# Performance work log

Measured on AMD Instinct MI355X. Metric: run time of the kernel, lower is better.

The kernel has to match this reference:

```python
import jax, jax.numpy as jnp
import numpy as np

B, C, N = 4, 512, 4096
CH = C // 2  # query/key projection dim


def setup_inputs() -> dict:
    key = jax.random.key(0)
    ks = jax.random.split(key, 10)
    s = 1.0 / np.sqrt(C)
    return {
        "Q": jax.random.normal(ks[0], (B, C, N), dtype=jnp.float32),
        "K": jax.random.normal(ks[1], (B, C, N), dtype=jnp.float32),
        "V": jax.random.normal(ks[2], (B, C, N), dtype=jnp.float32),
        "Wq": jax.random.normal(ks[3], (CH, C), dtype=jnp.float32) * s,
        "bq": jax.random.normal(ks[4], (CH,), dtype=jnp.float32) * s,
        "Wk": jax.random.normal(ks[5], (CH, C), dtype=jnp.float32) * s,
        "bk": jax.random.normal(ks[6], (CH,), dtype=jnp.float32) * s,
        "Wv": jax.random.normal(ks[7], (C, C), dtype=jnp.float32) * s,
        "bv": jax.random.normal(ks[8], (C,), dtype=jnp.float32) * s,
        "gamma": jnp.full((1,), 0.5, dtype=jnp.float32),  # torch inits to 0; nonzero for meaningful math
    }


def reference(Q, K, V, Wq, bq, Wk, bk, Wv, bv, gamma):
    # Conv1d(kernel_size=1) == per-position linear over channels
    q = jnp.einsum("oc,bcn->bon", Wq, Q) + bq[None, :, None]  # [B, C/2, N]
    k = jnp.einsum("oc,bcn->bon", Wk, K) + bk[None, :, None]  # [B, C/2, N]
    v = jnp.einsum("oc,bcn->bon", Wv, V) + bv[None, :, None]  # [B, C, N]
    # energy[b,n,m] = <q[b,:,n], k[b,:,m]>  (no 1/sqrt(d) scaling in original)
    energy = jnp.einsum("bcn,bcm->bnm", q, k)                 # [B, N, N]
    attention = jax.nn.softmax(energy, axis=-1)
    # out[b,c,n] = sum_m v[b,c,m] * attention[b,n,m]
    out = jnp.einsum("bcm,bnm->bcn", v, attention)            # [B, C, N]
    return gamma * out + V
```

## Files before the change

### kernel.cpp

```cpp
#include <hip/hip_runtime.h>
#include <cstdint>
#include <cstddef>

constexpr int B_  = 4;
constexpr int C_  = 512;
constexpr int CH_ = 256;
constexpr int N_  = 4096;
#define LOG2E 1.4426950408889634f

typedef float    f32x4 __attribute__((ext_vector_type(4)));
typedef _Float16 f16x8 __attribute__((ext_vector_type(8)));
typedef _Float16 f16x4 __attribute__((ext_vector_type(4)));

__device__ __forceinline__ f32x4 MFMA16(f16x8 a, f16x8 b, f32x4 c) {
  return __builtin_amdgcn_mfma_f32_16x16x32_f16(a, b, c, 0, 0, 0);
}

typedef const __attribute__((address_space(1))) unsigned int* gas_u32p;
typedef __attribute__((address_space(3))) unsigned int* las_u32p;
__device__ __forceinline__ void async16(const void* g, void* l) {
  __builtin_amdgcn_global_load_lds((gas_u32p)g, (las_u32p)l, 16, 0, 0);
}

template <int CTRL>
__device__ __forceinline__ float dppmax(float x) {
  float y = __builtin_bit_cast(
      float, __builtin_amdgcn_update_dpp(0, __builtin_bit_cast(int, x), CTRL,
                                         0xF, 0xF, true));
  return fmaxf(x, y);
}
__device__ __forceinline__ float rowmax16(float x) {
  x = dppmax<0x128>(x); x = dppmax<0x124>(x);
  x = dppmax<0x122>(x); x = dppmax<0x121>(x);
  return x;
}

__global__ void prep_w_kernel(const float* __restrict__ Wq,
                              const float* __restrict__ Wk,
                              const float* __restrict__ Wv,
                              _Float16* __restrict__ wq,
                              _Float16* __restrict__ wk,
                              _Float16* __restrict__ wv) {
  int i = blockIdx.x * 256 + threadIdx.x;
  if (i < CH_ * C_) {
    wq[i] = (_Float16)(Wq[i] * LOG2E);
    wk[i] = (_Float16)Wk[i];
  }
  if (i < C_ * C_) wv[i] = (_Float16)Wv[i];
}

__global__ __launch_bounds__(512, 4) void proj_kernel(
    const _Float16* __restrict__ wq, const _Float16* __restrict__ wk,
    const _Float16* __restrict__ wv, const float* __restrict__ Q,
    const float* __restrict__ K, const float* __restrict__ V,
    const float* __restrict__ bq, const float* __restrict__ bk,
    const float* __restrict__ bv, _Float16* __restrict__ qT,
    _Float16* __restrict__ kT, _Float16* __restrict__ vT) {
  __shared__ __align__(16) _Float16 lW[2][256 * 32];
  __shared__ __align__(16) _Float16 lX[2][64 * 56];

  const int y = blockIdx.y;
  const _Float16* W;
  const float* X;
  const float* bias;
  _Float16* out;
  int o0 = 0, M, mode;
  float bscale = 1.0f;
  if (y == 0) {
    W = wq; X = Q; bias = bq; out = qT; M = CH_; mode = 0; bscale = LOG2E;
  } else if (y == 1) {
    W = wk; X = K; bias = bk; out = kT; M = CH_; mode = 0;
  } else {
    W = wv; X = V; bias = bv; out = vT; M = C_; mode = 1; o0 = (y - 2) * 256;
  }

  const int tid = threadIdx.x;
  const int lane = tid & 63, wave = tid >> 6;
  const int g = lane >> 4, lm = lane & 15;
  const int b = blockIdx.z;
  const int n0 = blockIdx.x * 64;
  const int wo = (wave >> 1) * 64, wn = (wave & 1) * 32;

  const _Float16* Wb = W + (size_t)o0 * C_;
  const float* Xb = X + (size_t)b * C_ * N_;

  f32x4 acc[8];
#pragma unroll
  for (int i = 0; i < 8; ++i) acc[i] = f32x4{0.f, 0.f, 0.f, 0.f};

  auto stageW = [&](int s, int buf) {
    int c0 = s * 32;
#pragma unroll
    for (int r = 0; r < 2; ++r) {
      int ci = r * 512 + tid;
      int o = ci >> 2, cg = ci & 3;
      async16(Wb + (size_t)o * C_ + c0 + cg * 8,
              (char*)&lW[buf][0] + r * 8192 + wave * 1024);
    }
  };

  const int xc = tid >> 4;
  const int xn4 = (tid & 15) * 4;
  const int xgran = xc >> 3, xcin = xc & 7;
  auto gloadX = [&](int s) {
    return *(const f32x4*)(Xb + (size_t)(s * 32 + xc) * N_ + n0 + xn4);
  };
  auto writeX = [&](int buf, f32x4 v) {
#pragma unroll
    for (int i = 0; i < 4; ++i) {
      int n = xn4 + i;
      int pos = (xgran ^ ((n >> 2) & 3)) * 8 + xcin;
      lX[buf][n * 56 + pos] = (_Float16)v[i];
    }
  };

  f32x4 xg = gloadX(0);
  writeX(0, xg);
  xg = gloadX(1);
  stageW(0, 0);
  __syncthreads();

#pragma unroll
  for (int s = 0; s < 16; ++s) {
    const int cb = s & 1, nb = cb ^ 1;
    if (s < 15) stageW(s + 1, nb);
    f32x4 xgn;
    if (s < 14) xgn = gloadX(s + 2);

    f16x8 wf[4], xf[2];
#pragma unroll
    for (int ot = 0; ot < 4; ++ot)
      wf[ot] = *(const f16x8*)&lW[cb][((wo + ot * 16 + lm) * 4 + g) * 8];
#pragma unroll
    for (int nt = 0; nt < 2; ++nt) {
      int n = wn + nt * 16 + lm;
      int pos = (g ^ ((n >> 2) & 3)) * 8;
      xf[nt] = *(const f16x8*)&lX[cb][n * 56 + pos];
    }

    if (mode == 0) {
#pragma unroll
      for (int nt = 0; nt < 2; ++nt)
#pragma unroll
        for (int ot = 0; ot < 4; ++ot)
          acc[nt * 4 + ot] = MFMA16(xf[nt], wf[ot], acc[nt * 4 + ot]);
    } else {
#pragma unroll
      for (int ot = 0; ot < 4; ++ot)
#pragma unroll
        for (int nt = 0; nt < 2; ++nt)
          acc[ot * 2 + nt] = MFMA16(wf[ot], xf[nt], acc[ot * 2 + nt]);
    }

    if (s < 15) writeX(nb, xg);
    if (s < 14) xg = xgn;
    __syncthreads();
  }

  if (mode == 0) {
#pragma unroll
    for (int nt = 0; nt < 2; ++nt) {
#pragma unroll
      for (int ot = 0; ot < 4; ++ot) {
        int o = wo + ot * 16 + lm;
        float bv_ = bias[o] * bscale;
#pragma unroll
        for (int r = 0; r < 4; ++r) {
          int n = n0 + wn + nt * 16 + g * 4 + r;
          out[((size_t)b * N_ + n) * M + o] =
              (_Float16)(acc[nt * 4 + ot][r] + bv_);
        }
      }
    }
  } else {
#pragma unroll
    for (int ot = 0; ot < 4; ++ot) {
#pragma unroll
      for (int r = 0; r < 4; ++r) {
        int o = o0 + wo + ot * 16 + g * 4 + r;
        float bv_ = bias[o];
#pragma unroll
        for (int nt = 0; nt < 2; ++nt) {
          int n = n0 + wn + nt * 16 + lm;
          out[((size_t)b * M + o) * N_ + n] =
              (_Float16)(acc[ot * 2 + nt][r] + bv_);
        }
      }
    }
  }
}

__global__ __launch_bounds__(512, 2) void attn_kernel(
    const _Float16* __restrict__ qT, const _Float16* __restrict__ kT,
    const _Float16* __restrict__ vT, float* __restrict__ Op0,
    _Float16* __restrict__ Op1, float* __restrict__ mbuf,
    float* __restrict__ lbuf) {
  __shared__ __align__(16) _Float16 kstage[2 * 8192];
  __shared__ __align__(16) _Float16 P_t[128 * 72];
  __shared__ float al_st[128];
  __shared__ int bumped[8];

  const int tid = threadIdx.x;
  const int lane = tid & 63, wave = tid >> 6;
  const int g = lane >> 4, lm = lane & 15;

  const int bx = blockIdx.x;
  const int xcd = bx & 7;
  const int b = xcd >> 1, h = xcd & 1;
  const int n0 = (bx >> 3) * 128;
  const int mbase = h * 2048;
  const int c0w = wave * 64;

  f32x4 O[4][8];
#pragma unroll
  for (int i = 0; i < 4; ++i)
#pragma unroll
    for (int j = 0; j < 8; ++j) O[i][j] = f32x4{0.f, 0.f, 0.f, 0.f};
  f32x4 Ol = f32x4{0.f, 0.f, 0.f, 0.f};

  const _Float16* qTb = qT + ((size_t)b * N_ + n0) * CH_;
  f16x8 qf[8];
#pragma unroll
  for (int p = 0; p < 2; ++p) {
#pragma unroll
    for (int r = 0; r < 4; ++r) {
      int sidx = r * 512 + tid;
      int rl = sidx >> 5, cgs = sidx & 31;
      async16(qTb + (size_t)(p * 64 + rl) * CH_ + ((cgs ^ (rl & 7)) * 8),
              (char*)kstage + r * 8192 + wave * 1024);
    }
    __syncthreads();
    if ((wave >> 2) == p) {
      int rl = (wave & 3) * 16 + lm;
#pragma unroll
      for (int ks = 0; ks < 8; ++ks)
        qf[ks] =
            *(const f16x8*)&kstage[rl * 256 + (((ks * 4 + g) ^ (rl & 7)) * 8)];
    }
    __syncthreads();
  }

  const _Float16* kTb = kT + ((size_t)b * N_ + mbase) * CH_;
  auto stage_k = [&](int it) {
    int m0 = it * 32;
    char* dst0 = (char*)kstage + (it & 1) * 16384;
#pragma unroll
    for (int r = 0; r < 2; ++r) {
      int sidx = r * 512 + tid;
      int key = sidx >> 5, cgs = sidx & 31;
      async16(kTb + (size_t)(m0 + key) * CH_ + ((cgs ^ (key & 7)) * 8),
              dst0 + r * 8192 + wave * 1024);
    }
  };
  stage_k(0);

  const _Float16* vTb = vT + (size_t)b * C_ * N_ + mbase;
  const _Float16* vbase[4];
#pragma unroll
  for (int ct = 0; ct < 4; ++ct)
    vbase[ct] = vTb + (size_t)(c0w + ct * 16 + lm) * N_ + g * 8;
  f16x8 vf[4], vfn[4];
#pragma unroll
  for (int ct = 0; ct < 4; ++ct) vf[ct] = *(const f16x8*)vbase[ct];

  f32x4 m_run = f32x4{-1e30f, -1e30f, -1e30f, -1e30f};
  f16x8 ones;
#pragma unroll
  for (int i = 0; i < 8; ++i) ones[i] = (_Float16)1.0f;

#pragma unroll 1
  for (int it = 0; it < 64; ++it) {
    __syncthreads();
    if (it < 63) stage_k(it + 1);

    const _Float16* kb = kstage + (it & 1) * 8192;
    f32x4 s0 = f32x4{0.f, 0.f, 0.f, 0.f};
    f32x4 s1 = f32x4{0.f, 0.f, 0.f, 0.f};
    const int key0 = lm, key1 = 16 + lm;
#pragma unroll
    for (int ks = 0; ks < 8; ++ks) {
      f16x8 kf0 =
          *(const f16x8*)&kb[key0 * 256 + (((ks * 4 + g) ^ (key0 & 7)) * 8)];
      f16x8 kf1 =
          *(const f16x8*)&kb[key1 * 256 + (((ks * 4 + g) ^ (key1 & 7)) * 8)];
      s0 = MFMA16(qf[ks], kf0, s0);
      s1 = MFMA16(qf[ks], kf1, s1);
    }

    f32x4 alpha;
    bool anyb = false;
#pragma unroll
    for (int r = 0; r < 4; ++r) {
      float mx = rowmax16(fmaxf(s0[r], s1[r]));
      float mnew = fmaxf(m_run[r], mx);
      alpha[r] = exp2f(m_run[r] - mnew);
      anyb |= (mnew > m_run[r]);
      m_run[r] = mnew;
      float p0 = exp2f(s0[r] - mnew);
      float p1 = exp2f(s1[r] - mnew);
      int row = wave * 16 + g * 4 + r;
      P_t[row * 72 + lm] = (_Float16)p0;
      P_t[row * 72 + 16 + lm] = (_Float16)p1;
    }
    if (lm == 0) *(f32x4*)&al_st[wave * 16 + g * 4] = alpha;
    unsigned long long bal = __ballot(anyb);
    if (lane == 0) bumped[wave] = (bal != 0ull) ? 1 : 0;
    __syncthreads();

    if (it < 63) {
      int mo = (it + 1) * 32;
#pragma unroll
      for (int ct = 0; ct < 4; ++ct)
        vfn[ct] = *(const f16x8*)(vbase[ct] + mo);
    }

#pragma unroll
    for (int nt = 0; nt < 8; ++nt) {
      if (__builtin_amdgcn_readfirstlane(bumped[nt])) {
        float a = al_st[nt * 16 + lm];
#pragma unroll
        for (int ct = 0; ct < 4; ++ct) {
          O[ct][nt][0] *= a; O[ct][nt][1] *= a;
          O[ct][nt][2] *= a; O[ct][nt][3] *= a;
        }
      }
    }
    if (__builtin_amdgcn_readfirstlane(bumped[wave])) {
      float a = al_st[wave * 16 + lm];
      Ol[0] *= a; Ol[1] *= a; Ol[2] *= a; Ol[3] *= a;
    }

#pragma unroll
    for (int nt = 0; nt < 8; ++nt) {
      f16x8 pf = *(const f16x8*)&P_t[(nt * 16 + lm) * 72 + g * 8];
#pragma unroll
      for (int ct = 0; ct < 4; ++ct) O[ct][nt] = MFMA16(vf[ct], pf, O[ct][nt]);
    }
    {
      f16x8 pfo = *(const f16x8*)&P_t[(wave * 16 + lm) * 72 + g * 8];
      Ol = MFMA16(ones, pfo, Ol);
    }
    if (it < 63) {
#pragma unroll
      for (int ct = 0; ct < 4; ++ct) vf[ct] = vfn[ct];
    }
  }

  const size_t hb = (size_t)(b * 2 + h) * N_ + n0;
  if (lm == 0) {
#pragma unroll
    for (int r = 0; r < 4; ++r) mbuf[hb + wave * 16 + g * 4 + r] = m_run[r];
  }
  if (lane < 16) lbuf[hb + wave * 16 + lane] = Ol[0];

  if (h == 0) {
    float* ob = Op0 + (size_t)b * C_ * N_;
#pragma unroll
    for (int nt = 0; nt < 8; ++nt) {
      int n_g = n0 + nt * 16 + lm;
#pragma unroll
      for (int ct = 0; ct < 4; ++ct) {
        int cb = c0w + ct * 16 + g * 4;
#pragma unroll
        for (int r = 0; r < 4; ++r)
          ob[(size_t)(cb + r) * N_ + n_g] = O[ct][nt][r];
      }
    }
  } else {
    _Float16* ob = Op1 + (size_t)b * C_ * N_;
#pragma unroll
    for (int nt = 0; nt < 8; ++nt) {
      int n_g = n0 + nt * 16 + lm;
#pragma unroll
      for (int ct = 0; ct < 4; ++ct) {
        int cb = c0w + ct * 16 + g * 4;
#pragma unroll
        for (int r = 0; r < 4; ++r)
          ob[(size_t)(cb + r) * N_ + n_g] = (_Float16)O[ct][nt][r];
      }
    }
  }
}

__global__ __launch_bounds__(256) void combine_kernel(
    float* __restrict__ out, const _Float16* __restrict__ Op1,
    const float* __restrict__ mbuf, const float* __restrict__ lbuf,
    const float* __restrict__ Vin, const float* __restrict__ gptr) {
  const int b = blockIdx.y;
  const int tid = threadIdx.x;
  const int n = blockIdx.x * 64 + (tid & 15) * 4;
  const int cg = tid >> 4;
  const float gamma = gptr[0];

  float s0[4], s1[4];
#pragma unroll
  for (int j = 0; j < 4; ++j) {
    float m0 = mbuf[(size_t)(b * 2 + 0) * N_ + n + j];
    float m1 = mbuf[(size_t)(b * 2 + 1) * N_ + n + j];
    float mx = fmaxf(m0, m1);
    float a0 = exp2f(m0 - mx), a1 = exp2f(m1 - mx);
    float l = a0 * lbuf[(size_t)(b * 2 + 0) * N_ + n + j] +
              a1 * lbuf[(size_t)(b * 2 + 1) * N_ + n + j];
    float inv = gamma / l;
    s0[j] = a0 * inv;
    s1[j] = a1 * inv;
  }

  const _Float16* O1b = Op1 + (size_t)b * C_ * N_;
  for (int c = cg * 32; c < cg * 32 + 32; ++c) {
    size_t idx = ((size_t)b * C_ + c) * N_ + n;
    f32x4 p0 = *(const f32x4*)(out + idx);
    f16x4 p1 = *(const f16x4*)(O1b + (size_t)c * N_ + n);
    f32x4 V = *(const f32x4*)(Vin + idx);
    f32x4 r;
#pragma unroll
    for (int j = 0; j < 4; ++j)
      r[j] = p0[j] * s0[j] + (float)p1[j] * s1[j] + V[j];
    *(f32x4*)(out + idx) = r;
  }
}

extern "C" void kernel_launch(void* const* d_in, const int* in_sizes, int n_in,
                              void* d_out, int out_size, void* d_ws, size_t ws_size,
                              hipStream_t stream) {
  const float* Q  = (const float*)d_in[0];
  const float* K  = (const float*)d_in[1];
  const float* V  = (const float*)d_in[2];
  const float* Wq = (const float*)d_in[3];
  const float* bq = (const float*)d_in[4];
  const float* Wk = (const float*)d_in[5];
  const float* bk = (const float*)d_in[6];
  const float* Wv = (const float*)d_in[7];
  const float* bv = (const float*)d_in[8];
  const float* gm = (const float*)d_in[9];
  float* out = (float*)d_out;

  char* p = (char*)d_ws;
  _Float16* wq = (_Float16*)p; p += (size_t)CH_ * C_ * 2;
  _Float16* wk = (_Float16*)p; p += (size_t)CH_ * C_ * 2;
  _Float16* wv = (_Float16*)p; p += (size_t)C_ * C_ * 2;
  _Float16* qT = (_Float16*)p; p += (size_t)B_ * N_ * CH_ * 2;
  _Float16* kT = (_Float16*)p; p += (size_t)B_ * N_ * CH_ * 2;
  _Float16* vT = (_Float16*)p; p += (size_t)B_ * C_ * N_ * 2;
  _Float16* Op1 = (_Float16*)p; p += (size_t)B_ * C_ * N_ * 2;
  float* mbuf = (float*)p; p += (size_t)B_ * 2 * N_ * 4;
  float* lbuf = (float*)p; p += (size_t)B_ * 2 * N_ * 4;

  prep_w_kernel<<<(C_ * C_) / 256, 256, 0, stream>>>(Wq, Wk, Wv, wq, wk, wv);

  proj_kernel<<<dim3(N_ / 64, 4, B_), 512, 0, stream>>>(
      wq, wk, wv, Q, K, V, bq, bk, bv, qT, kT, vT);

  attn_kernel<<<256, 512, 0, stream>>>(qT, kT, vT, out, Op1, mbuf, lbuf);

  combine_kernel<<<dim3(N_ / 64, B_), 256, 0, stream>>>(out, Op1, mbuf, lbuf,
                                                        V, gm);
}
```

Baseline: 378.5 us.

## Retile attention to 64-query blocks of four waves with lazy max rescaling

The attention kernel now uses 256-thread blocks that each cover 64 query rows, launched as 512 blocks instead of 256. Each wave owns 128 output channels rather than 64. The V register prefetch for the next step is replaced by a direct load in the current iteration. The running-max update only rescales when the new max exceeds the old one by more than 8 (log2 domain), which skips most O rescales. It also wraps the MFMA sections in s_setprio. The cost is more K staging traffic per query, because each K tile is shared by fewer rows, exposed V load latency, and larger unnormalized exponent values that stay within fp16 range.

```diff
diff --git a/kernel.cpp b/kernel.cpp
--- a/kernel.cpp
+++ b/kernel.cpp
@@ -190,15 +190,15 @@
   }
 }
 
-__global__ __launch_bounds__(512, 2) void attn_kernel(
+__global__ __launch_bounds__(256, 2) void attn_kernel(
     const _Float16* __restrict__ qT, const _Float16* __restrict__ kT,
     const _Float16* __restrict__ vT, float* __restrict__ Op0,
     _Float16* __restrict__ Op1, float* __restrict__ mbuf,
     float* __restrict__ lbuf) {
   __shared__ __align__(16) _Float16 kstage[2 * 8192];
-  __shared__ __align__(16) _Float16 P_t[128 * 72];
-  __shared__ float al_st[128];
-  __shared__ int bumped[8];
+  __shared__ __align__(16) _Float16 P_t[64 * 72];
+  __shared__ float al_st[64];
+  __shared__ int bumped[4];
 
   const int tid = threadIdx.x;
   const int lane = tid & 63, wave = tid >> 6;
@@ -207,61 +207,55 @@
   const int bx = blockIdx.x;
   const int xcd = bx & 7;
   const int b = xcd >> 1, h = xcd & 1;
-  const int n0 = (bx >> 3) * 128;
+  const int n0 = (bx >> 3) * 64;
   const int mbase = h * 2048;
-  const int c0w = wave * 64;
-
-  f32x4 O[4][8];
-#pragma unroll
-  for (int i = 0; i < 4; ++i)
-#pragma unroll
-    for (int j = 0; j < 8; ++j) O[i][j] = f32x4{0.f, 0.f, 0.f, 0.f};
+  const int c0w = wave * 128;
+
+  f32x4 O[8][4];
+#pragma unroll
+  for (int i = 0; i < 8; ++i)
+#pragma unroll
+    for (int j = 0; j < 4; ++j) O[i][j] = f32x4{0.f, 0.f, 0.f, 0.f};
   f32x4 Ol = f32x4{0.f, 0.f, 0.f, 0.f};
 
   const _Float16* qTb = qT + ((size_t)b * N_ + n0) * CH_;
   f16x8 qf[8];
 #pragma unroll
-  for (int p = 0; p < 2; ++p) {
-#pragma unroll
-    for (int r = 0; r < 4; ++r) {
-      int sidx = r * 512 + tid;
-      int rl = sidx >> 5, cgs = sidx & 31;
-      async16(qTb + (size_t)(p * 64 + rl) * CH_ + ((cgs ^ (rl & 7)) * 8),
-              (char*)kstage + r * 8192 + wave * 1024);
-    }
-    __syncthreads();
-    if ((wave >> 2) == p) {
-      int rl = (wave & 3) * 16 + lm;
-#pragma unroll
-      for (int ks = 0; ks < 8; ++ks)
-        qf[ks] =
-            *(const f16x8*)&kstage[rl * 256 + (((ks * 4 + g) ^ (rl & 7)) * 8)];
-    }
-    __syncthreads();
-  }
+  for (int r = 0; r < 8; ++r) {
+    int sidx = r * 256 + tid;
+    int rl = sidx >> 5, cgs = sidx & 31;
+    async16(qTb + (size_t)rl * CH_ + ((cgs ^ (rl & 7)) * 8),
+            (char*)kstage + r * 4096 + wave * 1024);
+  }
+  __syncthreads();
+  {
+    int rl = wave * 16 + lm;
+#pragma unroll
+    for (int ks = 0; ks < 8; ++ks)
+      qf[ks] =
+          *(const f16x8*)&kstage[rl * 256 + (((ks * 4 + g) ^ (rl & 7)) * 8)];
+  }
+  __syncthreads();
 
   const _Float16* kTb = kT + ((size_t)b * N_ + mbase) * CH_;
   auto stage_k = [&](int it) {
     int m0 = it * 32;
     char* dst0 = (char*)kstage + (it & 1) * 16384;
 #pragma unroll
-    for (int r = 0; r < 2; ++r) {
-      int sidx = r * 512 + tid;
+    for (int r = 0; r < 4; ++r) {
+      int sidx = r * 256 + tid;
       int key = sidx >> 5, cgs = sidx & 31;
       async16(kTb + (size_t)(m0 + key) * CH_ + ((cgs ^ (key & 7)) * 8),
-              dst0 + r * 8192 + wave * 1024);
+              dst0 + r * 4096 + wave * 1024);
     }
   };
   stage_k(0);
 
   const _Float16* vTb = vT + (size_t)b * C_ * N_ + mbase;
-  const _Float16* vbase[4];
-#pragma unroll
-  for (int ct = 0; ct < 4; ++ct)
-    vbase[ct] = vTb + (size_t)(c0w + ct * 16 + lm) * N_ + g * 8;
-  f16x8 vf[4], vfn[4];
-#pragma unroll
-  for (int ct = 0; ct < 4; ++ct) vf[ct] = *(const f16x8*)vbase[ct];
+  int voff[8];
+#pragma unroll
+  for (int ct = 0; ct < 8; ++ct) voff[ct] = (c0w + ct * 16 + lm) * N_ + g * 8;
+  f16x8 vf[8];
 
   f32x4 m_run = f32x4{-1e30f, -1e30f, -1e30f, -1e30f};
   f16x8 ones;
@@ -277,6 +271,7 @@
     f32x4 s0 = f32x4{0.f, 0.f, 0.f, 0.f};
     f32x4 s1 = f32x4{0.f, 0.f, 0.f, 0.f};
     const int key0 = lm, key1 = 16 + lm;
+    __builtin_amdgcn_s_setprio(1);
 #pragma unroll
     for (int ks = 0; ks < 8; ++ks) {
       f16x8 kf0 =
@@ -286,15 +281,17 @@
       s0 = MFMA16(qf[ks], kf0, s0);
       s1 = MFMA16(qf[ks], kf1, s1);
     }
+    __builtin_amdgcn_s_setprio(0);
 
     f32x4 alpha;
     bool anyb = false;
 #pragma unroll
     for (int r = 0; r < 4; ++r) {
       float mx = rowmax16(fmaxf(s0[r], s1[r]));
-      float mnew = fmaxf(m_run[r], mx);
-      alpha[r] = exp2f(m_run[r] - mnew);
-      anyb |= (mnew > m_run[r]);
+      bool need = (mx > m_run[r] + 8.0f);
+      float mnew = need ? mx : m_run[r];
+      alpha[r] = need ? exp2f(m_run[r] - mnew) : 1.0f;
+      anyb |= need;
       m_run[r] = mnew;
       float p0 = exp2f(s0[r] - mnew);
       float p1 = exp2f(s1[r] - mnew);
@@ -307,19 +304,17 @@
     if (lane == 0) bumped[wave] = (bal != 0ull) ? 1 : 0;
     __syncthreads();
 
-    if (it < 63) {
-      int mo = (it + 1) * 32;
-#pragma unroll
-      for (int ct = 0; ct < 4; ++ct)
-        vfn[ct] = *(const f16x8*)(vbase[ct] + mo);
-    }
-
-#pragma unroll
-    for (int nt = 0; nt < 8; ++nt) {
+    const int mo = it * 32;
+#pragma unroll
+    for (int ct = 0; ct < 8; ++ct)
+      vf[ct] = *(const f16x8*)(vTb + voff[ct] + mo);
+
+#pragma unroll
+    for (int nt = 0; nt < 4; ++nt) {
       if (__builtin_amdgcn_readfirstlane(bumped[nt])) {
         float a = al_st[nt * 16 + lm];
 #pragma unroll
-        for (int ct = 0; ct < 4; ++ct) {
+        for (int ct = 0; ct < 8; ++ct) {
           O[ct][nt][0] *= a; O[ct][nt][1] *= a;
           O[ct][nt][2] *= a; O[ct][nt][3] *= a;
         }
@@ -330,20 +325,18 @@
       Ol[0] *= a; Ol[1] *= a; Ol[2] *= a; Ol[3] *= a;
     }
 
-#pragma unroll
-    for (int nt = 0; nt < 8; ++nt) {
+    __builtin_amdgcn_s_setprio(1);
+#pragma unroll
+    for (int nt = 0; nt < 4; ++nt) {
       f16x8 pf = *(const f16x8*)&P_t[(nt * 16 + lm) * 72 + g * 8];
 #pragma unroll
-      for (int ct = 0; ct < 4; ++ct) O[ct][nt] = MFMA16(vf[ct], pf, O[ct][nt]);
+      for (int ct = 0; ct < 8; ++ct) O[ct][nt] = MFMA16(vf[ct], pf, O[ct][nt]);
     }
     {
       f16x8 pfo = *(const f16x8*)&P_t[(wave * 16 + lm) * 72 + g * 8];
       Ol = MFMA16(ones, pfo, Ol);
     }
-    if (it < 63) {
-#pragma unroll
-      for (int ct = 0; ct < 4; ++ct) vf[ct] = vfn[ct];
-    }
+    __builtin_amdgcn_s_setprio(0);
   }
 
   const size_t hb = (size_t)(b * 2 + h) * N_ + n0;
@@ -356,10 +349,10 @@
   if (h == 0) {
     float* ob = Op0 + (size_t)b * C_ * N_;
 #pragma unroll
-    for (int nt = 0; nt < 8; ++nt) {
+    for (int nt = 0; nt < 4; ++nt) {
       int n_g = n0 + nt * 16 + lm;
 #pragma unroll
-      for (int ct = 0; ct < 4; ++ct) {
+      for (int ct = 0; ct < 8; ++ct) {
         int cb = c0w + ct * 16 + g * 4;
 #pragma unroll
         for (int r = 0; r < 4; ++r)
@@ -369,10 +362,10 @@
   } else {
     _Float16* ob = Op1 + (size_t)b * C_ * N_;
 #pragma unroll
-    for (int nt = 0; nt < 8; ++nt) {
+    for (int nt = 0; nt < 4; ++nt) {
       int n_g = n0 + nt * 16 + lm;
 #pragma unroll
-      for (int ct = 0; ct < 4; ++ct) {
+      for (int ct = 0; ct < 8; ++ct) {
         int cb = c0w + ct * 16 + g * 4;
 #pragma unroll
         for (int r = 0; r < 4; ++r)
@@ -451,7 +444,7 @@
   proj_kernel<<<dim3(N_ / 64, 4, B_), 512, 0, stream>>>(
       wq, wk, wv, Q, K, V, bq, bk, bv, qT, kT, vT);
 
-  attn_kernel<<<256, 512, 0, stream>>>(qT, kT, vT, out, Op1, mbuf, lbuf);
+  attn_kernel<<<512, 256, 0, stream>>>(qT, kT, vT, out, Op1, mbuf, lbuf);
 
   combine_kernel<<<dim3(N_ / 64, B_), 256, 0, stream>>>(out, Op1, mbuf, lbuf,
                                                         V, gm);
```

Result: no change. 384.9 us (+1.7%).

## Software-pipeline attention loop: overlap PV of previous tile with QK of current

Applied to the files above, without the earlier changes.

Double-buffers the P, alpha and bump-flag shared arrays so the PV MFMA for the previous key tile runs after the current tile's QK and softmax. This removes one __syncthreads per iteration and adds a drain step after the loop. It also adds a lazy max-rescale threshold, so the running max is only updated when the new max exceeds it by 8 in log2 units, and s_setprio hints around the MFMA blocks. The lazy rescale could risk fp16 overflow of P values, since they can reach up to 2^8 before being rescaled.

```diff
diff --git a/kernel.cpp b/kernel.cpp
--- a/kernel.cpp
+++ b/kernel.cpp
@@ -196,9 +196,9 @@
     _Float16* __restrict__ Op1, float* __restrict__ mbuf,
     float* __restrict__ lbuf) {
   __shared__ __align__(16) _Float16 kstage[2 * 8192];
-  __shared__ __align__(16) _Float16 P_t[128 * 72];
-  __shared__ float al_st[128];
-  __shared__ int bumped[8];
+  __shared__ __align__(16) _Float16 P_t[2][128 * 72];
+  __shared__ float al_st[2][128];
+  __shared__ int bumped[2][8];
 
   const int tid = threadIdx.x;
   const int lane = tid & 63, wave = tid >> 6;
@@ -255,13 +255,10 @@
   stage_k(0);
 
   const _Float16* vTb = vT + (size_t)b * C_ * N_ + mbase;
-  const _Float16* vbase[4];
-#pragma unroll
-  for (int ct = 0; ct < 4; ++ct)
-    vbase[ct] = vTb + (size_t)(c0w + ct * 16 + lm) * N_ + g * 8;
+  int voff[4];
+#pragma unroll
+  for (int ct = 0; ct < 4; ++ct) voff[ct] = (c0w + ct * 16 + lm) * N_ + g * 8;
   f16x8 vf[4], vfn[4];
-#pragma unroll
-  for (int ct = 0; ct < 4; ++ct) vf[ct] = *(const f16x8*)vbase[ct];
 
   f32x4 m_run = f32x4{-1e30f, -1e30f, -1e30f, -1e30f};
   f16x8 ones;
@@ -273,10 +270,15 @@
     __syncthreads();
     if (it < 63) stage_k(it + 1);
 
+#pragma unroll
+    for (int ct = 0; ct < 4; ++ct)
+      vfn[ct] = *(const f16x8*)(vTb + voff[ct] + it * 32);
+
     const _Float16* kb = kstage + (it & 1) * 8192;
     f32x4 s0 = f32x4{0.f, 0.f, 0.f, 0.f};
     f32x4 s1 = f32x4{0.f, 0.f, 0.f, 0.f};
     const int key0 = lm, key1 = 16 + lm;
+    __builtin_amdgcn_s_setprio(1);
 #pragma unroll
     for (int ks = 0; ks < 8; ++ks) {
       f16x8 kf0 =
@@ -286,38 +288,77 @@
       s0 = MFMA16(qf[ks], kf0, s0);
       s1 = MFMA16(qf[ks], kf1, s1);
     }
-
+    __builtin_amdgcn_s_setprio(0);
+
+    float p0v[4], p1v[4];
     f32x4 alpha;
     bool anyb = false;
 #pragma unroll
     for (int r = 0; r < 4; ++r) {
       float mx = rowmax16(fmaxf(s0[r], s1[r]));
-      float mnew = fmaxf(m_run[r], mx);
-      alpha[r] = exp2f(m_run[r] - mnew);
-      anyb |= (mnew > m_run[r]);
+      bool need = (mx > m_run[r] + 8.0f);
+      float mnew = need ? mx : m_run[r];
+      alpha[r] = need ? exp2f(m_run[r] - mnew) : 1.0f;
+      anyb |= need;
       m_run[r] = mnew;
-      float p0 = exp2f(s0[r] - mnew);
-      float p1 = exp2f(s1[r] - mnew);
+      p0v[r] = exp2f(s0[r] - mnew);
+      p1v[r] = exp2f(s1[r] - mnew);
+    }
+
+    const int pb = (it ^ 1) & 1;
+    if (it) {
+#pragma unroll
+      for (int nt = 0; nt < 8; ++nt) {
+        if (__builtin_amdgcn_readfirstlane(bumped[pb][nt])) {
+          float a = al_st[pb][nt * 16 + lm];
+#pragma unroll
+          for (int ct = 0; ct < 4; ++ct) {
+            O[ct][nt][0] *= a; O[ct][nt][1] *= a;
+            O[ct][nt][2] *= a; O[ct][nt][3] *= a;
+          }
+        }
+      }
+      if (__builtin_amdgcn_readfirstlane(bumped[pb][wave])) {
+        float a = al_st[pb][wave * 16 + lm];
+        Ol[0] *= a; Ol[1] *= a; Ol[2] *= a; Ol[3] *= a;
+      }
+      __builtin_amdgcn_s_setprio(1);
+#pragma unroll
+      for (int nt = 0; nt < 8; ++nt) {
+        f16x8 pf = *(const f16x8*)&P_t[pb][(nt * 16 + lm) * 72 + g * 8];
+#pragma unroll
+        for (int ct = 0; ct < 4; ++ct)
+          O[ct][nt] = MFMA16(vf[ct], pf, O[ct][nt]);
+      }
+      {
+        f16x8 pfo = *(const f16x8*)&P_t[pb][(wave * 16 + lm) * 72 + g * 8];
+        Ol = MFMA16(ones, pfo, Ol);
+      }
+      __builtin_amdgcn_s_setprio(0);
+    }
+
+    const int cb = it & 1;
+#pragma unroll
+    for (int r = 0; r < 4; ++r) {
       int row = wave * 16 + g * 4 + r;
-      P_t[row * 72 + lm] = (_Float16)p0;
-      P_t[row * 72 + 16 + lm] = (_Float16)p1;
-    }
-    if (lm == 0) *(f32x4*)&al_st[wave * 16 + g * 4] = alpha;
+      P_t[cb][row * 72 + lm] = (_Float16)p0v[r];
+      P_t[cb][row * 72 + 16 + lm] = (_Float16)p1v[r];
+    }
+    if (lm == 0) *(f32x4*)&al_st[cb][wave * 16 + g * 4] = alpha;
     unsigned long long bal = __ballot(anyb);
-    if (lane == 0) bumped[wave] = (bal != 0ull) ? 1 : 0;
-    __syncthreads();
-
-    if (it < 63) {
-      int mo = (it + 1) * 32;
-#pragma unroll
-      for (int ct = 0; ct < 4; ++ct)
-        vfn[ct] = *(const f16x8*)(vbase[ct] + mo);
-    }
-
+    if (lane == 0) bumped[cb][wave] = (bal != 0ull) ? 1 : 0;
+
+#pragma unroll
+    for (int ct = 0; ct < 4; ++ct) vf[ct] = vfn[ct];
+  }
+
+  __syncthreads();
+  {
+    const int pb = 1;
 #pragma unroll
     for (int nt = 0; nt < 8; ++nt) {
-      if (__builtin_amdgcn_readfirstlane(bumped[nt])) {
-        float a = al_st[nt * 16 + lm];
+      if (__builtin_amdgcn_readfirstlane(bumped[pb][nt])) {
+        float a = al_st[pb][nt * 16 + lm];
 #pragma unroll
         for (int ct = 0; ct < 4; ++ct) {
           O[ct][nt][0] *= a; O[ct][nt][1] *= a;
@@ -325,24 +366,20 @@
         }
       }
     }
-    if (__builtin_amdgcn_readfirstlane(bumped[wave])) {
-      float a = al_st[wave * 16 + lm];
+    if (__builtin_amdgcn_readfirstlane(bumped[pb][wave])) {
+      float a = al_st[pb][wave * 16 + lm];
       Ol[0] *= a; Ol[1] *= a; Ol[2] *= a; Ol[3] *= a;
     }
-
 #pragma unroll
     for (int nt = 0; nt < 8; ++nt) {
-      f16x8 pf = *(const f16x8*)&P_t[(nt * 16 + lm) * 72 + g * 8];
-#pragma unroll
-      for (int ct = 0; ct < 4; ++ct) O[ct][nt] = MFMA16(vf[ct], pf, O[ct][nt]);
+      f16x8 pf = *(const f16x8*)&P_t[pb][(nt * 16 + lm) * 72 + g * 8];
+#pragma unroll
+      for (int ct = 0; ct < 4; ++ct)
+        O[ct][nt] = MFMA16(vf[ct], pf, O[ct][nt]);
     }
     {
-      f16x8 pfo = *(const f16x8*)&P_t[(wave * 16 + lm) * 72 + g * 8];
+      f16x8 pfo = *(const f16x8*)&P_t[pb][(wave * 16 + lm) * 72 + g * 8];
       Ol = MFMA16(ones, pfo, Ol);
-    }
-    if (it < 63) {
-#pragma unroll
-      for (int ct = 0; ct < 4; ++ct) vf[ct] = vfn[ct];
     }
   }
 
@@ -360,10 +397,10 @@
       int n_g = n0 + nt * 16 + lm;
 #pragma unroll
       for (int ct = 0; ct < 4; ++ct) {
-        int cb = c0w + ct * 16 + g * 4;
+        int cb2 = c0w + ct * 16 + g * 4;
 #pragma unroll
         for (int r = 0; r < 4; ++r)
-          ob[(size_t)(cb + r) * N_ + n_g] = O[ct][nt][r];
+          ob[(size_t)(cb2 + r) * N_ + n_g] = O[ct][nt][r];
       }
     }
   } else {
@@ -373,10 +410,10 @@
       int n_g = n0 + nt * 16 + lm;
 #pragma unroll
       for (int ct = 0; ct < 4; ++ct) {
-        int cb = c0w + ct * 16 + g * 4;
+        int cb2 = c0w + ct * 16 + g * 4;
 #pragma unroll
         for (int r = 0; r < 4; ++r)
-          ob[(size_t)(cb + r) * N_ + n_g] = (_Float16)O[ct][nt][r];
+          ob[(size_t)(cb2 + r) * N_ + n_g] = (_Float16)O[ct][nt][r];
       }
     }
   }
```

Result: slower. 402.1 us (+6.2%).

## Transpose score MFMA and use lazy thresholded max rescaling in softmax

Applied to the files above, without the earlier changes.

The QK^T MFMA operands are swapped so each lane holds scores for a single query row. The row max then reduces in-lane plus two cross-lane shuffles instead of DPP row reductions, and P is written to LDS as packed f16x4. The running max is now only raised when the new max exceeds the old one by more than 8 (log2 units), which skips most O rescales. Unnormalized probabilities can reach up to 2^8 in fp16, which costs some precision headroom in exchange for fewer rescaling passes.

```diff
diff --git a/kernel.cpp b/kernel.cpp
--- a/kernel.cpp
+++ b/kernel.cpp
@@ -20,19 +20,6 @@
 typedef __attribute__((address_space(3))) unsigned int* las_u32p;
 __device__ __forceinline__ void async16(const void* g, void* l) {
   __builtin_amdgcn_global_load_lds((gas_u32p)g, (las_u32p)l, 16, 0, 0);
-}
-
-template <int CTRL>
-__device__ __forceinline__ float dppmax(float x) {
-  float y = __builtin_bit_cast(
-      float, __builtin_amdgcn_update_dpp(0, __builtin_bit_cast(int, x), CTRL,
-                                         0xF, 0xF, true));
-  return fmaxf(x, y);
-}
-__device__ __forceinline__ float rowmax16(float x) {
-  x = dppmax<0x128>(x); x = dppmax<0x124>(x);
-  x = dppmax<0x122>(x); x = dppmax<0x121>(x);
-  return x;
 }
 
 __global__ void prep_w_kernel(const float* __restrict__ Wq,
@@ -263,7 +250,7 @@
 #pragma unroll
   for (int ct = 0; ct < 4; ++ct) vf[ct] = *(const f16x8*)vbase[ct];
 
-  f32x4 m_run = f32x4{-1e30f, -1e30f, -1e30f, -1e30f};
+  float m_run = -1e30f;
   f16x8 ones;
 #pragma unroll
   for (int i = 0; i < 8; ++i) ones[i] = (_Float16)1.0f;
@@ -283,27 +270,29 @@
           *(const f16x8*)&kb[key0 * 256 + (((ks * 4 + g) ^ (key0 & 7)) * 8)];
       f16x8 kf1 =
           *(const f16x8*)&kb[key1 * 256 + (((ks * 4 + g) ^ (key1 & 7)) * 8)];
-      s0 = MFMA16(qf[ks], kf0, s0);
-      s1 = MFMA16(qf[ks], kf1, s1);
-    }
-
-    f32x4 alpha;
-    bool anyb = false;
+      s0 = MFMA16(kf0, qf[ks], s0);
+      s1 = MFMA16(kf1, qf[ks], s1);
+    }
+
+    float mx = fmaxf(fmaxf(fmaxf(s0[0], s0[1]), fmaxf(s0[2], s0[3])),
+                     fmaxf(fmaxf(s1[0], s1[1]), fmaxf(s1[2], s1[3])));
+    mx = fmaxf(mx, __shfl_xor(mx, 16));
+    mx = fmaxf(mx, __shfl_xor(mx, 32));
+    bool need = (mx > m_run + 8.0f);
+    float mnew = need ? mx : m_run;
+    float alpha = need ? exp2f(m_run - mnew) : 1.0f;
+    m_run = mnew;
+    f16x4 pa, pb;
 #pragma unroll
     for (int r = 0; r < 4; ++r) {
-      float mx = rowmax16(fmaxf(s0[r], s1[r]));
-      float mnew = fmaxf(m_run[r], mx);
-      alpha[r] = exp2f(m_run[r] - mnew);
-      anyb |= (mnew > m_run[r]);
-      m_run[r] = mnew;
-      float p0 = exp2f(s0[r] - mnew);
-      float p1 = exp2f(s1[r] - mnew);
-      int row = wave * 16 + g * 4 + r;
-      P_t[row * 72 + lm] = (_Float16)p0;
-      P_t[row * 72 + 16 + lm] = (_Float16)p1;
-    }
-    if (lm == 0) *(f32x4*)&al_st[wave * 16 + g * 4] = alpha;
-    unsigned long long bal = __ballot(anyb);
+      pa[r] = (_Float16)exp2f(s0[r] - mnew);
+      pb[r] = (_Float16)exp2f(s1[r] - mnew);
+    }
+    const int prow = wave * 16 + lm;
+    *(f16x4*)&P_t[prow * 72 + g * 4] = pa;
+    *(f16x4*)&P_t[prow * 72 + 16 + g * 4] = pb;
+    if (g == 0) al_st[prow] = alpha;
+    unsigned long long bal = __ballot(need);
     if (lane == 0) bumped[wave] = (bal != 0ull) ? 1 : 0;
     __syncthreads();
 
@@ -347,10 +336,7 @@
   }
 
   const size_t hb = (size_t)(b * 2 + h) * N_ + n0;
-  if (lm == 0) {
-#pragma unroll
-    for (int r = 0; r < 4; ++r) mbuf[hb + wave * 16 + g * 4 + r] = m_run[r];
-  }
+  if (g == 0) mbuf[hb + wave * 16 + lm] = m_run;
   if (lane < 16) lbuf[hb + wave * 16 + lane] = Ol[0];
 
   if (h == 0) {
```

New measurement: 357.7 us. 5.5% less time.
